# Performance work log

Hardware: AMD Instinct MI355X
Metric: run time of the kernel (lower is better)

The kernel has to match this reference:

```python
import jax, jax.numpy as jnp
import numpy as np

IN_FEATURES = 4096
OUT_FEATURES = 11008
GROUP_SIZE = 32
M_TOKENS = 32
Q_MID = 8  # int4 midpoint: dequant = (q - 8) * scale + zero


def setup_inputs() -> dict:
    key = jax.random.key(0)
    k1, k2, k3, k4 = jax.random.split(key, 4)
    n_groups = IN_FEATURES // GROUP_SIZE
    inputs = {
        "input": jax.random.normal(k1, (M_TOKENS, IN_FEATURES), dtype=jnp.float32),
        "weight": jax.random.randint(k2, (OUT_FEATURES, IN_FEATURES), 0, 16, dtype=jnp.int32),
        "scales_and_zeros": jax.random.normal(k3, (n_groups, OUT_FEATURES, 2), dtype=jnp.float32),
        "bias": jax.random.normal(k4, (OUT_FEATURES,), dtype=jnp.float32),
        "group_size": GROUP_SIZE,
    }
    return inputs


def reference(input, weight, scales_and_zeros, bias, group_size):
    out_features, in_features = weight.shape
    n_groups = in_features // group_size
    # scales/zeros per (group, out) -> [out, n_groups]
    scale = scales_and_zeros[..., 0].T  # [out, G]
    zero = scales_and_zeros[..., 1].T   # [out, G]
    # dequantize int4 weight: w = (q - 8) * scale + zero, per group along in_features
    q = weight.astype(jnp.float32).reshape(out_features, n_groups, group_size)
    w_fp = (q - Q_MID) * scale[:, :, None] + zero[:, :, None]  # [out, G, gs]
    w_fp = w_fp.reshape(out_features, in_features)
    # y = x @ W^T + b
    y = jnp.einsum("bi,oi->bo", input, w_fp) + bias
    return y
```

## Files before the change

kernel.cpp:

```cpp
#include <hip/hip_runtime.h>
#include <hip/hip_bf16.h>
#include <stdint.h>

#define M_TOK 32
#define IN_F 4096
#define OUT_F 11008
#define NSPLIT 8
#define KRANGE (IN_F / NSPLIT)

typedef __attribute__((ext_vector_type(8))) short bf16x8;
typedef __attribute__((ext_vector_type(4))) float f32x4;

__device__ inline uint32_t pack_bf16(float a, float b) {
    __hip_bfloat16 ha = __float2bfloat16(a);
    __hip_bfloat16 hb = __float2bfloat16(b);
    uint16_t ua = *(uint16_t*)&ha;
    uint16_t ub = *(uint16_t*)&hb;
    return (uint32_t)ua | ((uint32_t)ub << 16);
}

__global__ void init_out_kernel(const float* __restrict__ bias, float* __restrict__ out) {
    int o = blockIdx.x * 256 + threadIdx.x;
    int m = blockIdx.y;
    out[(size_t)m * OUT_F + o] = bias[o];
}

__launch_bounds__(256)
__global__ void qgemm_kernel(const float* __restrict__ x,
                             const int* __restrict__ wq,
                             const float* __restrict__ sz,
                             float* __restrict__ out) {
    const int bid = blockIdx.x;
    const int ks  = bid & (NSPLIT - 1);
    const int nb  = bid >> 3;
    const int t   = threadIdx.x;
    const int wv  = t >> 6;
    const int l   = t & 63;
    const int lm  = l & 15;
    const int lq  = l >> 4;

    const int row = nb * 64 + wv * 16 + lm;
    const int k0  = ks * KRANGE;

    const int*   wp  = wq + (size_t)row * IN_F + k0 + lq * 8;
    const float* xp0 = x + (size_t)lm * IN_F + k0 + lq * 8;
    const float* xp1 = xp0 + (size_t)16 * IN_F;
    const float* szp = sz + ((size_t)(k0 >> 5) * OUT_F + row) * 2;

    f32x4 acc0 = {0.f, 0.f, 0.f, 0.f};
    f32x4 acc1 = {0.f, 0.f, 0.f, 0.f};

    #pragma unroll 4
    for (int s = 0; s < KRANGE / 32; ++s) {
        int4   q0 = *(const int4*)(wp);
        int4   q1 = *(const int4*)(wp + 4);
        float2 sv = *(const float2*)(szp);
        float4 xa = *(const float4*)(xp0);
        float4 xb = *(const float4*)(xp0 + 4);
        float4 xc = *(const float4*)(xp1);
        float4 xd = *(const float4*)(xp1 + 4);
        wp  += 32;
        xp0 += 32;
        xp1 += 32;
        szp += (size_t)OUT_F * 2;

        const float sc = sv.x;
        const float zp = sv.y - 8.0f * sv.x;

        union { bf16x8 v; uint32_t u[4]; } bf, a0, a1;
        bf.u[0] = pack_bf16((float)q0.x * sc + zp, (float)q0.y * sc + zp);
        bf.u[1] = pack_bf16((float)q0.z * sc + zp, (float)q0.w * sc + zp);
        bf.u[2] = pack_bf16((float)q1.x * sc + zp, (float)q1.y * sc + zp);
        bf.u[3] = pack_bf16((float)q1.z * sc + zp, (float)q1.w * sc + zp);
        a0.u[0] = pack_bf16(xa.x, xa.y);
        a0.u[1] = pack_bf16(xa.z, xa.w);
        a0.u[2] = pack_bf16(xb.x, xb.y);
        a0.u[3] = pack_bf16(xb.z, xb.w);
        a1.u[0] = pack_bf16(xc.x, xc.y);
        a1.u[1] = pack_bf16(xc.z, xc.w);
        a1.u[2] = pack_bf16(xd.x, xd.y);
        a1.u[3] = pack_bf16(xd.z, xd.w);

        acc0 = __builtin_amdgcn_mfma_f32_16x16x32_bf16(a0.v, bf.v, acc0, 0, 0, 0);
        acc1 = __builtin_amdgcn_mfma_f32_16x16x32_bf16(a1.v, bf.v, acc1, 0, 0, 0);
    }

    const int ocol = nb * 64 + wv * 16 + lm;
    #pragma unroll
    for (int i = 0; i < 4; ++i) {
        int m0 = lq * 4 + i;
        atomicAdd(&out[(size_t)m0 * OUT_F + ocol], acc0[i]);
        atomicAdd(&out[(size_t)(16 + m0) * OUT_F + ocol], acc1[i]);
    }
}

extern "C" void kernel_launch(void* const* d_in, const int* in_sizes, int n_in,
                              void* d_out, int out_size, void* d_ws, size_t ws_size,
                              hipStream_t stream) {
    const float* x    = (const float*)d_in[0];
    const int*   wq   = (const int*)d_in[1];
    const float* sz   = (const float*)d_in[2];
    const float* bias = (const float*)d_in[3];
    float* out = (float*)d_out;

    dim3 gi(OUT_F / 256, M_TOK);
    init_out_kernel<<<gi, 256, 0, stream>>>(bias, out);

    dim3 gg((OUT_F / 64) * NSPLIT);
    qgemm_kernel<<<gg, 256, 0, stream>>>(x, wq, sz, out);
}
```

Before: 277.8 us.

## Double-buffer weight tiles in LDS via direct global-to-LDS loads

Weight tiles are now staged into a two-buffer LDS array with global_load_lds, using an XOR-swizzled column layout. The next k-step's tile is prefetched while the current one is dequantized and fed to MFMA. The goal is to hide global-load latency on the large int32 weight stream, which was previously loaded directly into registers. In exchange it adds a block barrier every k-step and relies on that barrier to wait for the async LDS writes.

```diff
diff --git a/kernel.cpp b/kernel.cpp
--- a/kernel.cpp
+++ b/kernel.cpp
@@ -7,6 +7,7 @@
 #define OUT_F 11008
 #define NSPLIT 8
 #define KRANGE (IN_F / NSPLIT)
+#define NSTEP  (KRANGE / 32)
 
 typedef __attribute__((ext_vector_type(8))) short bf16x8;
 typedef __attribute__((ext_vector_type(4))) float f32x4;
@@ -30,6 +31,8 @@
                              const int* __restrict__ wq,
                              const float* __restrict__ sz,
                              float* __restrict__ out) {
+    __shared__ int lds_w[2][64 * 32];
+
     const int bid = blockIdx.x;
     const int ks  = bid & (NSPLIT - 1);
     const int nb  = bid >> 3;
@@ -39,10 +42,30 @@
     const int lm  = l & 15;
     const int lq  = l >> 4;
 
-    const int row = nb * 64 + wv * 16 + lm;
-    const int k0  = ks * KRANGE;
+    const int row0 = nb * 64;
+    const int row  = row0 + wv * 16 + lm;
+    const int k0   = ks * KRANGE;
 
-    const int*   wp  = wq + (size_t)row * IN_F + k0 + lq * 8;
+    const int rs    = t >> 3;
+    const int cs    = t & 7;
+    const int* gw0  = wq + (size_t)(row0 + rs) * IN_F + k0 + ((cs ^ (rs & 7)) * 4);
+    const int* gw1  = gw0 + (size_t)32 * IN_F;
+
+#define STAGE(buf, soff) do {                                                   \
+    __builtin_amdgcn_global_load_lds(                                           \
+        (const __attribute__((address_space(1))) int*)(gw0 + (soff)),           \
+        (__attribute__((address_space(3))) int*)&lds_w[(buf)][wv * 256],        \
+        16, 0, 0);                                                              \
+    __builtin_amdgcn_global_load_lds(                                           \
+        (const __attribute__((address_space(1))) int*)(gw1 + (soff)),           \
+        (__attribute__((address_space(3))) int*)&lds_w[(buf)][1024 + wv * 256], \
+        16, 0, 0);                                                              \
+} while (0)
+
+    const int rloc = wv * 16 + lm;
+    const int c0   = rloc * 32 + (((2 * lq)     ^ (rloc & 7)) * 4);
+    const int c1   = rloc * 32 + (((2 * lq + 1) ^ (rloc & 7)) * 4);
+
     const float* xp0 = x + (size_t)lm * IN_F + k0 + lq * 8;
     const float* xp1 = xp0 + (size_t)16 * IN_F;
     const float* szp = sz + ((size_t)(k0 >> 5) * OUT_F + row) * 2;
@@ -50,16 +73,20 @@
     f32x4 acc0 = {0.f, 0.f, 0.f, 0.f};
     f32x4 acc1 = {0.f, 0.f, 0.f, 0.f};
 
-    #pragma unroll 4
-    for (int s = 0; s < KRANGE / 32; ++s) {
-        int4   q0 = *(const int4*)(wp);
-        int4   q1 = *(const int4*)(wp + 4);
+    STAGE(0, 0);
+    int cur = 0;
+    #pragma unroll 2
+    for (int s = 0; s < NSTEP; ++s) {
+        __syncthreads();
+        if (s + 1 < NSTEP) STAGE(cur ^ 1, (s + 1) * 32);
+
+        int4   q0 = *(const int4*)(&lds_w[cur][c0]);
+        int4   q1 = *(const int4*)(&lds_w[cur][c1]);
         float2 sv = *(const float2*)(szp);
         float4 xa = *(const float4*)(xp0);
         float4 xb = *(const float4*)(xp0 + 4);
         float4 xc = *(const float4*)(xp1);
         float4 xd = *(const float4*)(xp1 + 4);
-        wp  += 32;
         xp0 += 32;
         xp1 += 32;
         szp += (size_t)OUT_F * 2;
@@ -83,9 +110,11 @@
 
         acc0 = __builtin_amdgcn_mfma_f32_16x16x32_bf16(a0.v, bf.v, acc0, 0, 0, 0);
         acc1 = __builtin_amdgcn_mfma_f32_16x16x32_bf16(a1.v, bf.v, acc1, 0, 0, 0);
+        cur ^= 1;
     }
+#undef STAGE
 
-    const int ocol = nb * 64 + wv * 16 + lm;
+    const int ocol = row;
     #pragma unroll
     for (int i = 0; i < 4; ++i) {
         int m0 = lq * 4 + i;
```

After: 273.9 us. About the same (-1.4%).
